# Kernel optimization log

Measured on AMD Instinct MI355X. Metric: run time of the kernel, lower is better.

Reference implementation:

```python
import jax, jax.numpy as jnp
import numpy as np

BN_EPS = 1e-5


def setup_inputs() -> dict:
    key = jax.random.key(0)
    k1, k2, k3 = jax.random.split(key, 3)
    B, C, H, W = 8, 1024, 48, 48
    Cb = 512
    x = jax.random.normal(k1, (B, C, H, W), dtype=jnp.float32)
    Wg = jax.random.normal(k2, (Cb, C), dtype=jnp.float32) * (1.0 / np.sqrt(C))
    Wz = jax.random.normal(k3, (C, Cb), dtype=jnp.float32) * (1.0 / np.sqrt(Cb))
    gamma = jnp.zeros((C,), dtype=jnp.float32)  # BN weight, const-init 0
    beta = jnp.zeros((C,), dtype=jnp.float32)   # BN bias,  const-init 0
    return {"x": x, "Wg": Wg, "Wz": Wz, "gamma": gamma, "beta": beta}


def reference(x, Wg, Wz, gamma, beta):
    B, C, H, W = x.shape
    HW = H * W
    xf = x.reshape(B, C, HW)                                  # [B,C,N]
    # attn[b,n,m] = <x[b,:,n], x[b,:,m]> / (H*W), softmax over m
    attn = jnp.einsum('bcn,bcm->bnm', xf, xf) / HW            # [B,N,N]
    attn = jax.nn.softmax(attn, axis=-1)
    # g: 1x1 conv C -> Cb (no bias)
    g = jnp.einsum('dc,bcn->bdn', Wg, xf)                     # [B,Cb,N]
    # y[b,d,n] = sum_m attn[b,n,m] * g[b,d,m]
    y = jnp.einsum('bnm,bdm->bdn', attn, g)                   # [B,Cb,N]
    # W_z: 1x1 conv Cb -> C (no bias)
    wy = jnp.einsum('cd,bdn->bcn', Wz, y)                     # [B,C,N]
    # BatchNorm2d in training mode: batch stats over (B, N), biased variance
    mean = jnp.mean(wy, axis=(0, 2), keepdims=True)
    var = jnp.mean(jnp.square(wy - mean), axis=(0, 2), keepdims=True)
    wy_bn = (wy - mean) * jax.lax.rsqrt(var + BN_EPS)
    wy_bn = wy_bn * gamma[None, :, None] + beta[None, :, None]
    z = wy_bn.reshape(B, C, H, W) + x
    return z
```

## Files before the change

kernel.cpp:

```cpp
#include <hip/hip_runtime.h>
#include <hip/hip_bf16.h>
#include <stdint.h>


typedef __bf16 bf16;
typedef __attribute__((ext_vector_type(8))) __bf16 bf16x8;
typedef __attribute__((ext_vector_type(4))) __bf16 bf16x4;
typedef __attribute__((ext_vector_type(4))) float f32x4;

template <bool F32OUT, bool BNRED, bool BXI>
__global__ __launch_bounds__(256)
void gemm_btz(const bf16* __restrict__ Ag, const bf16* __restrict__ Bg,
              void* __restrict__ Dg, int K, int N,
              long long sA, long long sB, long long sD, float alpha,
              float* __restrict__ ps, float* __restrict__ pq, int nInner, int nz)
{
    const int d  = blockIdx.x;
    const int zz = d % nz;
    const int t0 = d / nz;
    const int bI = t0 % nInner;
    const int bO = t0 / nInner;
    const int bx = BXI ? bI : bO;
    const int by = BXI ? bO : bI;

    __shared__ char lds[32768];
    char* ldsA = lds;
    char* ldsB = lds + 16384;

    const int lane = threadIdx.x & 63;
    const int wv   = threadIdx.x >> 6;
    const int wm   = wv >> 1;
    const int wn   = wv & 1;

    const bf16* Ab = Ag + (long long)zz * sA + (long long)by * 128 * K;
    const bf16* Bb = Bg + (long long)zz * sB + (long long)bx * 128 * K;

    f32x4 acc[4][4];
    #pragma unroll
    for (int i = 0; i < 4; ++i)
        #pragma unroll
        for (int j = 0; j < 4; ++j) {
            f32x4 z = {0.f, 0.f, 0.f, 0.f};
            acc[i][j] = z;
        }

    for (int k0 = 0; k0 < K; k0 += 64) {
        #pragma unroll
        for (int t = 0; t < 4; ++t) {
            int ch  = (wv * 4 + t) * 64 + lane;
            int row = ch >> 3;
            int cc  = (ch & 7) ^ (row & 7);
            bf16x8 va = *(const bf16x8*)(Ab + (long long)row * K + k0 + cc * 8);
            bf16x8 vb = *(const bf16x8*)(Bb + (long long)row * K + k0 + cc * 8);
            *(bf16x8*)(ldsA + ch * 16) = va;
            *(bf16x8*)(ldsB + ch * 16) = vb;
        }
        __syncthreads();

        #pragma unroll
        for (int kk = 0; kk < 64; kk += 32) {
            bf16x8 af[4], bfr[4];
            #pragma unroll
            for (int i = 0; i < 4; ++i) {
                int r = wm * 64 + i * 16 + (lane & 15);
                int c = ((kk >> 3) + (lane >> 4)) ^ (r & 7);
                af[i] = *(const bf16x8*)(ldsA + r * 128 + c * 16);
            }
            #pragma unroll
            for (int j = 0; j < 4; ++j) {
                int r = wn * 64 + j * 16 + (lane & 15);
                int c = ((kk >> 3) + (lane >> 4)) ^ (r & 7);
                bfr[j] = *(const bf16x8*)(ldsB + r * 128 + c * 16);
            }
            #pragma unroll
            for (int i = 0; i < 4; ++i)
                #pragma unroll
                for (int j = 0; j < 4; ++j)
                    acc[i][j] = __builtin_amdgcn_mfma_f32_16x16x32_bf16(af[i], bfr[j], acc[i][j], 0, 0, 0);
        }
        __syncthreads();
    }

    float* bs = (float*)lds;
    float* bq = (float*)(lds + 512);
    if (BNRED) {
        if (threadIdx.x < 128) { bs[threadIdx.x] = 0.f; bq[threadIdx.x] = 0.f; }
        __syncthreads();
    }

    const int m_base = by * 128 + wm * 64;
    const int n_base = bx * 128 + wn * 64;
    float s_it[4][4], q_it[4][4];
    #pragma unroll
    for (int i = 0; i < 4; ++i) {
        #pragma unroll
        for (int t = 0; t < 4; ++t) { s_it[i][t] = 0.f; q_it[i][t] = 0.f; }
    }
    #pragma unroll
    for (int i = 0; i < 4; ++i) {
        #pragma unroll
        for (int j = 0; j < 4; ++j) {
            int col = n_base + j * 16 + (lane & 15);
            #pragma unroll
            for (int t = 0; t < 4; ++t) {
                int rowg = m_base + i * 16 + (lane >> 4) * 4 + t;
                float v = acc[i][j][t] * alpha;
                if (F32OUT) ((float*)Dg)[(long long)zz * sD + (long long)rowg * N + col] = v;
                else        ((bf16*)Dg)[(long long)zz * sD + (long long)rowg * N + col] = (bf16)v;
                if (BNRED) { s_it[i][t] += v; q_it[i][t] += v * v; }
            }
        }
    }

    if (BNRED) {
        #pragma unroll
        for (int i = 0; i < 4; ++i) {
            #pragma unroll
            for (int t = 0; t < 4; ++t) {
                float s = s_it[i][t], q = q_it[i][t];
                #pragma unroll
                for (int m = 1; m < 16; m <<= 1) {
                    s += __shfl_xor(s, m);
                    q += __shfl_xor(q, m);
                }
                if ((lane & 15) == 0) {
                    int cl = wm * 64 + i * 16 + (lane >> 4) * 4 + t;
                    atomicAdd(&bs[cl], s);
                    atomicAdd(&bq[cl], q);
                }
            }
        }
        __syncthreads();
        if (threadIdx.x < 128) {
            int cg = by * 128 + threadIdx.x;
            atomicAdd(&ps[cg], bs[threadIdx.x]);
            atomicAdd(&pq[cg], bq[threadIdx.x]);
        }
    }
}

__global__ __launch_bounds__(256)
void gemm_sym(const bf16* __restrict__ Xg, bf16* __restrict__ Dg,
              int K, int N, long long sX, long long sD, float alpha)
{
    const int NZ = gridDim.z;
    const int d  = blockIdx.z * 171 + blockIdx.x;
    const int zz = d % NZ;
    int tlin     = d / NZ;
    int bi = 0;
    while (tlin >= 18 - bi) { tlin -= 18 - bi; ++bi; }
    const int bj = bi + tlin;
    const bool mir  = (bj > bi);
    const bool diag = (bj == bi);

    __shared__ __align__(16) char lds[35840];
    char* ldsA = lds;
    char* ldsB = diag ? lds : (lds + 16384);

    const int lane = threadIdx.x & 63;
    const int wv   = threadIdx.x >> 6;
    const int wm   = wv >> 1;
    const int wn   = wv & 1;

    const bf16* Ab = Xg + (long long)zz * sX + (long long)bi * 128 * K;
    const bf16* Bb = Xg + (long long)zz * sX + (long long)bj * 128 * K;

    f32x4 acc[4][4];
    #pragma unroll
    for (int i = 0; i < 4; ++i)
        #pragma unroll
        for (int j = 0; j < 4; ++j) {
            f32x4 z = {0.f, 0.f, 0.f, 0.f};
            acc[i][j] = z;
        }

    for (int k0 = 0; k0 < K; k0 += 64) {
        #pragma unroll
        for (int t = 0; t < 4; ++t) {
            int ch  = (wv * 4 + t) * 64 + lane;
            int row = ch >> 3;
            int cc  = (ch & 7) ^ (row & 7);
            bf16x8 va = *(const bf16x8*)(Ab + (long long)row * K + k0 + cc * 8);
            *(bf16x8*)(ldsA + ch * 16) = va;
            if (!diag) {
                bf16x8 vb = *(const bf16x8*)(Bb + (long long)row * K + k0 + cc * 8);
                *(bf16x8*)(ldsB + ch * 16) = vb;
            }
        }
        __syncthreads();

        #pragma unroll
        for (int kk = 0; kk < 64; kk += 32) {
            bf16x8 af[4], bfr[4];
            #pragma unroll
            for (int i = 0; i < 4; ++i) {
                int r = wm * 64 + i * 16 + (lane & 15);
                int c = ((kk >> 3) + (lane >> 4)) ^ (r & 7);
                af[i] = *(const bf16x8*)(ldsA + r * 128 + c * 16);
            }
            #pragma unroll
            for (int j = 0; j < 4; ++j) {
                int r = wn * 64 + j * 16 + (lane & 15);
                int c = ((kk >> 3) + (lane >> 4)) ^ (r & 7);
                bfr[j] = *(const bf16x8*)(ldsB + r * 128 + c * 16);
            }
            #pragma unroll
            for (int i = 0; i < 4; ++i)
                #pragma unroll
                for (int j = 0; j < 4; ++j)
                    acc[i][j] = __builtin_amdgcn_mfma_f32_16x16x32_bf16(af[i], bfr[j], acc[i][j], 0, 0, 0);
        }
        __syncthreads();
    }

    bf16* Db = Dg + (long long)zz * sD;
    bf16 (*tr)[140] = (bf16(*)[140])lds;

    #pragma unroll
    for (int i = 0; i < 4; ++i) {
        #pragma unroll
        for (int j = 0; j < 4; ++j) {
            int c_loc = wn * 64 + j * 16 + (lane & 15);
            int col   = bj * 128 + c_loc;
            bf16x4 tv;
            #pragma unroll
            for (int t = 0; t < 4; ++t) {
                int r_loc = wm * 64 + i * 16 + (lane >> 4) * 4 + t;
                float v = acc[i][j][t] * alpha;
                Db[(long long)(bi * 128 + r_loc) * N + col] = (bf16)v;
                tv[t] = (bf16)v;
            }
            if (mir) {
                int r_base = wm * 64 + i * 16 + (lane >> 4) * 4;
                *(bf16x4*)(&tr[c_loc][r_base]) = tv;
            }
        }
    }

    if (mir) {
        __syncthreads();
        const int cc = threadIdx.x >> 1, hf = threadIdx.x & 1;
        const bf16* src = &tr[cc][hf * 64];
        bf16* dst = Db + (long long)(bj * 128 + cc) * N + bi * 128 + hf * 64;
        #pragma unroll
        for (int j2 = 0; j2 < 8; ++j2)
            *(bf16x8*)(dst + j2 * 8) = *(const bf16x8*)(src + j2 * 8);
    }
}

__global__ __launch_bounds__(256)
void f32_to_bf16(const float* __restrict__ in, bf16* __restrict__ out, int n)
{
    int idx = (blockIdx.x * 256 + threadIdx.x) * 4;
    if (idx < n) {
        float4 v = *(const float4*)(in + idx);
        out[idx + 0] = (bf16)v.x;
        out[idx + 1] = (bf16)v.y;
        out[idx + 2] = (bf16)v.z;
        out[idx + 3] = (bf16)v.w;
    }
}

__global__ __launch_bounds__(256)
void zero_f32(float* __restrict__ p)
{
    p[blockIdx.x * 256 + threadIdx.x] = 0.f;
}

__global__ __launch_bounds__(256)
void transpose_f32_bf16(const float* __restrict__ x, bf16* __restrict__ xT)
{
    __shared__ bf16 tile[32][33];
    const float* xb = x + (long long)blockIdx.z * 1024 * 2304;
    bf16* xo = xT + (long long)blockIdx.z * 2304 * 1024;
    const int n0 = blockIdx.x * 32;
    const int c0 = blockIdx.y * 32;
    const int tx = threadIdx.x, ty = threadIdx.y;
    #pragma unroll
    for (int i = 0; i < 32; i += 8)
        tile[ty + i][tx] = (bf16)xb[(long long)(c0 + ty + i) * 2304 + n0 + tx];
    __syncthreads();
    #pragma unroll
    for (int i = 0; i < 32; i += 8)
        xo[(long long)(n0 + ty + i) * 1024 + c0 + tx] = tile[tx][ty + i];
}

__global__ __launch_bounds__(256)
void softmax_rows(bf16* __restrict__ S)
{
    bf16* p = S + (long long)blockIdx.x * 2304;
    const int t = threadIdx.x;
    __shared__ float red[256];

    bf16x8 v8 = *(const bf16x8*)(p + t * 8);
    float vt = (float)p[2048 + t];
    float f[8];
    float mx = vt;
    #pragma unroll
    for (int i = 0; i < 8; ++i) { f[i] = (float)v8[i]; mx = fmaxf(mx, f[i]); }

    red[t] = mx; __syncthreads();
    for (int s = 128; s > 0; s >>= 1) { if (t < s) red[t] = fmaxf(red[t], red[t + s]); __syncthreads(); }
    mx = red[0];
    __syncthreads();

    float sum = 0.f;
    #pragma unroll
    for (int i = 0; i < 8; ++i) { f[i] = __expf(f[i] - mx); sum += f[i]; }
    vt = __expf(vt - mx); sum += vt;

    red[t] = sum; __syncthreads();
    for (int s = 128; s > 0; s >>= 1) { if (t < s) red[t] += red[t + s]; __syncthreads(); }
    float inv = 1.0f / red[0];

    bf16x8 o;
    #pragma unroll
    for (int i = 0; i < 8; ++i) o[i] = (bf16)(f[i] * inv);
    *(bf16x8*)(p + t * 8) = o;
    p[2048 + t] = (bf16)(vt * inv);
}

__global__ __launch_bounds__(256)
void bn_finalize(const float* __restrict__ ps, const float* __restrict__ pq,
                 float* __restrict__ mean, float* __restrict__ istd)
{
    int c = blockIdx.x * 256 + threadIdx.x;
    float mu = ps[c] / 18432.0f;
    mean[c] = mu;
    istd[c] = rsqrtf(pq[c] / 18432.0f - mu * mu + 1e-5f);
}

__global__ __launch_bounds__(256)
void bn_apply_b(const bf16* __restrict__ wy, const float* __restrict__ x,
                const float* __restrict__ gamma, const float* __restrict__ beta,
                const float* __restrict__ mean, const float* __restrict__ istd,
                float* __restrict__ z)
{
    long long idx = ((long long)blockIdx.x * 256 + threadIdx.x) * 8;
    int c = (int)((idx / 2304) & 1023);
    float sc = gamma[c] * istd[c];
    float sh = beta[c] - mean[c] * sc;
    bf16x8 w  = *(const bf16x8*)(wy + idx);
    float4 x0 = *(const float4*)(x + idx);
    float4 x1 = *(const float4*)(x + idx + 4);
    float4 o0, o1;
    o0.x = (float)w[0] * sc + sh + x0.x;
    o0.y = (float)w[1] * sc + sh + x0.y;
    o0.z = (float)w[2] * sc + sh + x0.z;
    o0.w = (float)w[3] * sc + sh + x0.w;
    o1.x = (float)w[4] * sc + sh + x1.x;
    o1.y = (float)w[5] * sc + sh + x1.y;
    o1.z = (float)w[6] * sc + sh + x1.z;
    o1.w = (float)w[7] * sc + sh + x1.w;
    *(float4*)(z + idx)     = o0;
    *(float4*)(z + idx + 4) = o1;
}

extern "C" void kernel_launch(void* const* d_in, const int* in_sizes, int n_in,
                              void* d_out, int out_size, void* d_ws, size_t ws_size,
                              hipStream_t stream)
{
    const float* x     = (const float*)d_in[0];
    const float* Wg    = (const float*)d_in[1];
    const float* Wz    = (const float*)d_in[2];
    const float* gamma = (const float*)d_in[3];
    const float* beta  = (const float*)d_in[4];
    float* zo = (float*)d_out;

    const int B = 8, C = 1024, Cb = 512, N = 2304;

    const size_t fixedB = ((size_t)Cb * C * 2) * 2 + (size_t)C * 4 * 4 + 4096;
    const size_t perB   = ((size_t)N * C + (size_t)Cb * N + (size_t)N * N + (size_t)N * Cb
                           + (size_t)C * N) * 2 + 1280;
    int BC = 8;
    while (BC > 1 && fixedB + perB * (size_t)BC > ws_size) BC >>= 1;

    char* p = (char*)d_ws;
    auto alloc = [&](size_t bytes) { char* r = p; p += (bytes + 255) & ~(size_t)255; return r; };
    bf16*  Wgb  = (bf16*)alloc((size_t)Cb * C * 2);
    bf16*  Wzb  = (bf16*)alloc((size_t)C * Cb * 2);
    float* psum = (float*)alloc((size_t)C * 4);
    float* pqsm = (float*)alloc((size_t)C * 4);
    float* mean = (float*)alloc((size_t)C * 4);
    float* istd = (float*)alloc((size_t)C * 4);
    bf16*  xT   = (bf16*)alloc((size_t)BC * N * C * 2);
    bf16*  g    = (bf16*)alloc((size_t)BC * Cb * N * 2);
    bf16*  attn = (bf16*)alloc((size_t)BC * N * N * 2);
    bf16*  yT   = (bf16*)alloc((size_t)BC * N * Cb * 2);
    bf16*  wyb  = (bf16*)alloc((size_t)BC * C * N * 2);

    f32_to_bf16<<<dim3((Cb * C) / (256 * 4)), 256, 0, stream>>>(Wg, Wgb, Cb * C);
    f32_to_bf16<<<dim3((C * Cb) / (256 * 4)), 256, 0, stream>>>(Wz, Wzb, C * Cb);
    zero_f32<<<dim3(8), 256, 0, stream>>>(psum);

    for (int cs = 0; cs < B; cs += BC) {
        const float* xc = x + (long long)cs * C * N;

        transpose_f32_bf16<<<dim3(N / 32, C / 32, BC), dim3(32, 8), 0, stream>>>(xc, xT);

        gemm_btz<false, false, false><<<dim3(18 * 4 * BC), 256, 0, stream>>>(
            Wgb, xT, g, C, N, 0, (long long)N * C, (long long)Cb * N, 1.0f,
            nullptr, nullptr, 4, BC);

        gemm_sym<<<dim3(171, 1, BC), 256, 0, stream>>>(
            xT, attn, C, N, (long long)N * C, (long long)N * N, 1.0f / 2304.0f);

        softmax_rows<<<dim3(BC * N), 256, 0, stream>>>(attn);

        gemm_btz<false, false, true><<<dim3(4 * 18 * BC), 256, 0, stream>>>(
            attn, g, yT, N, Cb, (long long)N * N, (long long)Cb * N, (long long)N * Cb, 1.0f,
            nullptr, nullptr, 4, BC);

        gemm_btz<false, true, false><<<dim3(18 * 8 * BC), 256, 0, stream>>>(
            Wzb, yT, wyb + (long long)0, Cb, N, 0, (long long)N * Cb, (long long)C * N, 1.0f,
            psum, pqsm, 8, BC);

    }

    bn_finalize<<<dim3(C / 256), 256, 0, stream>>>(psum, pqsm, mean, istd);

    if (BC == B) {
        bn_apply_b<<<dim3((B * C * N) / (256 * 8)), 256, 0, stream>>>(
            wyb, x, gamma, beta, mean, istd, zo);
    } else {
        for (int cs = 0; cs < B; cs += BC) {
            const float* xc = x + (long long)cs * C * N;
            float* zoc = zo + (long long)cs * C * N;
            transpose_f32_bf16<<<dim3(N / 32, C / 32, BC), dim3(32, 8), 0, stream>>>(xc, xT);
            gemm_btz<false, false, false><<<dim3(18 * 4 * BC), 256, 0, stream>>>(
                Wgb, xT, g, C, N, 0, (long long)N * C, (long long)Cb * N, 1.0f,
                nullptr, nullptr, 4, BC);
            gemm_sym<<<dim3(171, 1, BC), 256, 0, stream>>>(
                xT, attn, C, N, (long long)N * C, (long long)N * N, 1.0f / 2304.0f);
            softmax_rows<<<dim3(BC * N), 256, 0, stream>>>(attn);
            gemm_btz<false, false, true><<<dim3(4 * 18 * BC), 256, 0, stream>>>(
                attn, g, yT, N, Cb, (long long)N * N, (long long)Cb * N, (long long)N * Cb,
                1.0f, nullptr, nullptr, 4, BC);
            gemm_btz<false, false, false><<<dim3(18 * 8 * BC), 256, 0, stream>>>(
                Wzb, yT, wyb, Cb, N, 0, (long long)N * Cb, (long long)C * N, 1.0f,
                nullptr, nullptr, 8, BC);
            bn_apply_b<<<dim3((BC * C * N) / (256 * 8)), 256, 0, stream>>>(
                wyb, xc, gamma, beta, mean, istd, zoc);
        }
    }
}
```

Measured before the change: 404.9 us.

## Fuse softmax into attention GEMM epilogue and defer normalization to next GEMM

Removes the standalone row-softmax kernel. The symmetric attention GEMM now writes exp(scaled score) directly and atomically accumulates row sums, using column sums for the mirrored tiles. The following attn×g GEMM divides the A operand by the row sum as it loads tiles into shared memory. This drops a full read-and-write pass over the N×N attention matrix, but it skips max subtraction, so it assumes the scores are small enough not to overflow exp. It also adds atomics, shrinks the transpose LDS tile (losing its padding), and sets occupancy hints through launch_bounds.

```diff
diff --git a/kernel.cpp b/kernel.cpp
--- a/kernel.cpp
+++ b/kernel.cpp
@@ -8,12 +8,13 @@
 typedef __attribute__((ext_vector_type(4))) __bf16 bf16x4;
 typedef __attribute__((ext_vector_type(4))) float f32x4;
 
-template <bool F32OUT, bool BNRED, bool BXI>
-__global__ __launch_bounds__(256)
+template <bool F32OUT, bool BNRED, bool BXI, bool SMAX>
+__global__ __launch_bounds__(256, 5)
 void gemm_btz(const bf16* __restrict__ Ag, const bf16* __restrict__ Bg,
               void* __restrict__ Dg, int K, int N,
               long long sA, long long sB, long long sD, float alpha,
-              float* __restrict__ ps, float* __restrict__ pq, int nInner, int nz)
+              float* __restrict__ ps, float* __restrict__ pq,
+              const float* __restrict__ rsum, long long sR, int nInner, int nz)
 {
     const int d  = blockIdx.x;
     const int zz = d % nz;
@@ -35,6 +36,15 @@
     const bf16* Ab = Ag + (long long)zz * sA + (long long)by * 128 * K;
     const bf16* Bb = Bg + (long long)zz * sB + (long long)bx * 128 * K;
 
+    float ainv[4];
+    if (SMAX) {
+        #pragma unroll
+        for (int t = 0; t < 4; ++t) {
+            int row = ((wv * 4 + t) * 64 + lane) >> 3;
+            ainv[t] = 1.0f / rsum[(long long)zz * sR + by * 128 + row];
+        }
+    }
+
     f32x4 acc[4][4];
     #pragma unroll
     for (int i = 0; i < 4; ++i)
@@ -52,6 +62,11 @@
             int cc  = (ch & 7) ^ (row & 7);
             bf16x8 va = *(const bf16x8*)(Ab + (long long)row * K + k0 + cc * 8);
             bf16x8 vb = *(const bf16x8*)(Bb + (long long)row * K + k0 + cc * 8);
+            if (SMAX) {
+                #pragma unroll
+                for (int q8 = 0; q8 < 8; ++q8)
+                    va[q8] = (bf16)((float)va[q8] * ainv[t]);
+            }
             *(bf16x8*)(ldsA + ch * 16) = va;
             *(bf16x8*)(ldsB + ch * 16) = vb;
         }
@@ -139,9 +154,10 @@
     }
 }
 
-__global__ __launch_bounds__(256)
+__global__ __launch_bounds__(256, 5)
 void gemm_sym(const bf16* __restrict__ Xg, bf16* __restrict__ Dg,
-              int K, int N, long long sX, long long sD, float alpha)
+              int K, int N, long long sX, long long sD, float alpha,
+              float* __restrict__ rsum)
 {
     const int NZ = gridDim.z;
     const int d  = blockIdx.z * 171 + blockIdx.x;
@@ -153,7 +169,7 @@
     const bool mir  = (bj > bi);
     const bool diag = (bj == bi);
 
-    __shared__ __align__(16) char lds[35840];
+    __shared__ __align__(16) char lds[32768];
     char* ldsA = lds;
     char* ldsB = diag ? lds : (lds + 16384);
 
@@ -214,7 +230,17 @@
     }
 
     bf16* Db = Dg + (long long)zz * sD;
-    bf16 (*tr)[140] = (bf16(*)[140])lds;
+    float* rs = rsum + (long long)zz * N;
+    bf16 (*tr)[128] = (bf16(*)[128])lds;
+
+    float rowsum[4][4];
+    float colsum[4];
+    #pragma unroll
+    for (int i = 0; i < 4; ++i)
+        #pragma unroll
+        for (int t = 0; t < 4; ++t) rowsum[i][t] = 0.f;
+    #pragma unroll
+    for (int j = 0; j < 4; ++j) colsum[j] = 0.f;
 
     #pragma unroll
     for (int i = 0; i < 4; ++i) {
@@ -226,9 +252,12 @@
             #pragma unroll
             for (int t = 0; t < 4; ++t) {
                 int r_loc = wm * 64 + i * 16 + (lane >> 4) * 4 + t;
-                float v = acc[i][j][t] * alpha;
-                Db[(long long)(bi * 128 + r_loc) * N + col] = (bf16)v;
-                tv[t] = (bf16)v;
+                float e = __expf(acc[i][j][t] * alpha);
+                bf16 eb = (bf16)e;
+                Db[(long long)(bi * 128 + r_loc) * N + col] = eb;
+                tv[t] = eb;
+                rowsum[i][t] += e;
+                colsum[j]    += e;
             }
             if (mir) {
                 int r_base = wm * 64 + i * 16 + (lane >> 4) * 4;
@@ -237,7 +266,25 @@
         }
     }
 
+    #pragma unroll
+    for (int i = 0; i < 4; ++i) {
+        #pragma unroll
+        for (int t = 0; t < 4; ++t) {
+            float s = rowsum[i][t];
+            s += __shfl_xor(s, 1); s += __shfl_xor(s, 2);
+            s += __shfl_xor(s, 4); s += __shfl_xor(s, 8);
+            if ((lane & 15) == 0)
+                atomicAdd(&rs[bi * 128 + wm * 64 + i * 16 + (lane >> 4) * 4 + t], s);
+        }
+    }
     if (mir) {
+        #pragma unroll
+        for (int j = 0; j < 4; ++j) {
+            float s = colsum[j];
+            s += __shfl_xor(s, 16); s += __shfl_xor(s, 32);
+            if (lane < 16)
+                atomicAdd(&rs[bj * 128 + wn * 64 + j * 16 + lane], s);
+        }
         __syncthreads();
         const int cc = threadIdx.x >> 1, hf = threadIdx.x & 1;
         const bf16* src = &tr[cc][hf * 64];
@@ -283,41 +330,6 @@
     #pragma unroll
     for (int i = 0; i < 32; i += 8)
         xo[(long long)(n0 + ty + i) * 1024 + c0 + tx] = tile[tx][ty + i];
-}
-
-__global__ __launch_bounds__(256)
-void softmax_rows(bf16* __restrict__ S)
-{
-    bf16* p = S + (long long)blockIdx.x * 2304;
-    const int t = threadIdx.x;
-    __shared__ float red[256];
-
-    bf16x8 v8 = *(const bf16x8*)(p + t * 8);
-    float vt = (float)p[2048 + t];
-    float f[8];
-    float mx = vt;
-    #pragma unroll
-    for (int i = 0; i < 8; ++i) { f[i] = (float)v8[i]; mx = fmaxf(mx, f[i]); }
-
-    red[t] = mx; __syncthreads();
-    for (int s = 128; s > 0; s >>= 1) { if (t < s) red[t] = fmaxf(red[t], red[t + s]); __syncthreads(); }
-    mx = red[0];
-    __syncthreads();
-
-    float sum = 0.f;
-    #pragma unroll
-    for (int i = 0; i < 8; ++i) { f[i] = __expf(f[i] - mx); sum += f[i]; }
-    vt = __expf(vt - mx); sum += vt;
-
-    red[t] = sum; __syncthreads();
-    for (int s = 128; s > 0; s >>= 1) { if (t < s) red[t] += red[t + s]; __syncthreads(); }
-    float inv = 1.0f / red[0];
-
-    bf16x8 o;
-    #pragma unroll
-    for (int i = 0; i < 8; ++i) o[i] = (bf16)(f[i] * inv);
-    *(bf16x8*)(p + t * 8) = o;
-    p[2048 + t] = (bf16)(vt * inv);
 }
 
 __global__ __launch_bounds__(256)
@@ -371,7 +383,7 @@
 
     const size_t fixedB = ((size_t)Cb * C * 2) * 2 + (size_t)C * 4 * 4 + 4096;
     const size_t perB   = ((size_t)N * C + (size_t)Cb * N + (size_t)N * N + (size_t)N * Cb
-                           + (size_t)C * N) * 2 + 1280;
+                           + (size_t)C * N) * 2 + (size_t)N * 4 + 1536;
     int BC = 8;
     while (BC > 1 && fixedB + perB * (size_t)BC > ws_size) BC >>= 1;
 
@@ -383,6 +395,7 @@
     float* pqsm = (float*)alloc((size_t)C * 4);
     float* mean = (float*)alloc((size_t)C * 4);
     float* istd = (float*)alloc((size_t)C * 4);
+    float* rsum = (float*)alloc((size_t)B * N * 4);
     bf16*  xT   = (bf16*)alloc((size_t)BC * N * C * 2);
     bf16*  g    = (bf16*)alloc((size_t)BC * Cb * N * 2);
     bf16*  attn = (bf16*)alloc((size_t)BC * N * N * 2);
@@ -398,23 +411,21 @@
 
         transpose_f32_bf16<<<dim3(N / 32, C / 32, BC), dim3(32, 8), 0, stream>>>(xc, xT);
 
-        gemm_btz<false, false, false><<<dim3(18 * 4 * BC), 256, 0, stream>>>(
+        gemm_btz<false, false, false, false><<<dim3(18 * 4 * BC), 256, 0, stream>>>(
             Wgb, xT, g, C, N, 0, (long long)N * C, (long long)Cb * N, 1.0f,
-            nullptr, nullptr, 4, BC);
-
+            nullptr, nullptr, nullptr, 0, 4, BC);
+
+        zero_f32<<<dim3(BC * 9), 256, 0, stream>>>(rsum);
         gemm_sym<<<dim3(171, 1, BC), 256, 0, stream>>>(
-            xT, attn, C, N, (long long)N * C, (long long)N * N, 1.0f / 2304.0f);
-
-        softmax_rows<<<dim3(BC * N), 256, 0, stream>>>(attn);
-
-        gemm_btz<false, false, true><<<dim3(4 * 18 * BC), 256, 0, stream>>>(
+            xT, attn, C, N, (long long)N * C, (long long)N * N, 1.0f / 2304.0f, rsum);
+
+        gemm_btz<false, false, true, true><<<dim3(4 * 18 * BC), 256, 0, stream>>>(
             attn, g, yT, N, Cb, (long long)N * N, (long long)Cb * N, (long long)N * Cb, 1.0f,
-            nullptr, nullptr, 4, BC);
-
-        gemm_btz<false, true, false><<<dim3(18 * 8 * BC), 256, 0, stream>>>(
-            Wzb, yT, wyb + (long long)0, Cb, N, 0, (long long)N * Cb, (long long)C * N, 1.0f,
-            psum, pqsm, 8, BC);
-
+            nullptr, nullptr, rsum, N, 4, BC);
+
+        gemm_btz<false, true, false, false><<<dim3(18 * 8 * BC), 256, 0, stream>>>(
+            Wzb, yT, wyb, Cb, N, 0, (long long)N * Cb, (long long)C * N, 1.0f,
+            psum, pqsm, nullptr, 0, 8, BC);
     }
 
     bn_finalize<<<dim3(C / 256), 256, 0, stream>>>(psum, pqsm, mean, istd);
@@ -427,18 +438,18 @@
             const float* xc = x + (long long)cs * C * N;
             float* zoc = zo + (long long)cs * C * N;
             transpose_f32_bf16<<<dim3(N / 32, C / 32, BC), dim3(32, 8), 0, stream>>>(xc, xT);
-            gemm_btz<false, false, false><<<dim3(18 * 4 * BC), 256, 0, stream>>>(
+            gemm_btz<false, false, false, false><<<dim3(18 * 4 * BC), 256, 0, stream>>>(
                 Wgb, xT, g, C, N, 0, (long long)N * C, (long long)Cb * N, 1.0f,
-                nullptr, nullptr, 4, BC);
+                nullptr, nullptr, nullptr, 0, 4, BC);
+            zero_f32<<<dim3(BC * 9), 256, 0, stream>>>(rsum);
             gemm_sym<<<dim3(171, 1, BC), 256, 0, stream>>>(
-                xT, attn, C, N, (long long)N * C, (long long)N * N, 1.0f / 2304.0f);
-            softmax_rows<<<dim3(BC * N), 256, 0, stream>>>(attn);
-            gemm_btz<false, false, true><<<dim3(4 * 18 * BC), 256, 0, stream>>>(
+                xT, attn, C, N, (long long)N * C, (long long)N * N, 1.0f / 2304.0f, rsum);
+            gemm_btz<false, false, true, true><<<dim3(4 * 18 * BC), 256, 0, stream>>>(
                 attn, g, yT, N, Cb, (long long)N * N, (long long)Cb * N, (long long)N * Cb,
-                1.0f, nullptr, nullptr, 4, BC);
-            gemm_btz<false, false, false><<<dim3(18 * 8 * BC), 256, 0, stream>>>(
+                1.0f, nullptr, nullptr, rsum, N, 4, BC);
+            gemm_btz<false, false, false, false><<<dim3(18 * 8 * BC), 256, 0, stream>>>(
                 Wzb, yT, wyb, Cb, N, 0, (long long)N * Cb, (long long)C * N, 1.0f,
-                nullptr, nullptr, 8, BC);
+                nullptr, nullptr, nullptr, 0, 8, BC);
             bn_apply_b<<<dim3((BC * C * N) / (256 * 8)), 256, 0, stream>>>(
                 wyb, xc, gamma, beta, mean, istd, zoc);
         }
```

New measurement: 635.7 us. 57.0% more time.
